# Kernel optimization log

Hardware: AMD Instinct MI355X
Metric: run time of the kernel (lower is better)

The kernel has to match this reference:

```python
import jax, jax.numpy as jnp
import numpy as np

V, D, H = 32000, 256, 1024
B, T = 64, 512


def setup_inputs() -> dict:
    key = jax.random.key(0)
    k1, k2, k3, k4 = jax.random.split(key, 4)
    inputs = jax.random.randint(k1, (B, T), 0, V, dtype=jnp.int64 if jax.config.jax_enable_x64 else jnp.int32)
    hidden_state = jnp.zeros((B, H), dtype=jnp.float32)
    embedding = jax.random.normal(k2, (V, D), dtype=jnp.float32) * 0.05
    kernel = jax.random.normal(k3, (D, 3 * H), dtype=jnp.float32) * (1.0 / np.sqrt(D))
    rec_kernel = jax.random.normal(k4, (H, 3 * H), dtype=jnp.float32) * (1.0 / np.sqrt(H))
    bias = jnp.zeros((2, 3 * H), dtype=jnp.float32)  # [input_bias; recurrent_bias] (reset_after=True)
    return {"inputs": inputs, "hidden_state": hidden_state, "embedding": embedding,
            "kernel": kernel, "rec_kernel": rec_kernel, "bias": bias}


def reference(inputs, hidden_state, embedding, kernel, rec_kernel, bias):
    # Embedding lookup: [B,T] -> [B,T,D]
    x = embedding[inputs]
    # Precompute all input projections for the whole sequence: [B,T,3H]
    x_proj = jnp.einsum('btd,dh->bth', x, kernel) + bias[0]

    def step(h, xp_t):
        # Keras GRU, reset_after=True (cuDNN-compatible gate ordering z,r,h)
        rec = h @ rec_kernel + bias[1]              # [B,3H]
        xz, xr, xh = jnp.split(xp_t, 3, axis=-1)
        rz, rr, rh = jnp.split(rec, 3, axis=-1)
        z = jax.nn.sigmoid(xz + rz)
        r = jax.nn.sigmoid(xr + rr)
        hh = jnp.tanh(xh + r * rh)
        h_new = z * h + (1.0 - z) * hh
        return h_new, h_new

    state, outs = jax.lax.scan(step, hidden_state, jnp.swapaxes(x_proj, 0, 1))
    outputs = jnp.swapaxes(outs, 0, 1)  # [B,T,H]
    return outputs, state
```

## Files before the change

kernel.cpp:

```cpp
#include <hip/hip_runtime.h>

#define Bb 64
#define Tt 512
#define Dd 256
#define Hh 1024
#define G3 3072

#define FLAG_BYTES 4096
#define HF_OFF     FLAG_BYTES

typedef __attribute__((ext_vector_type(8))) __bf16 bf16x8;
typedef __attribute__((ext_vector_type(4))) float f32x4;
typedef __attribute__((ext_vector_type(2))) unsigned long long u64x2;

static __device__ __forceinline__ f32x4 mfma16(bf16x8 a, bf16x8 b, f32x4 c){
    return __builtin_amdgcn_mfma_f32_16x16x32_bf16(a, b, c, 0, 0, 0);
}
static __device__ __forceinline__ unsigned short bfbits(__bf16 v){
    return __builtin_bit_cast(unsigned short, v);
}

__device__ __forceinline__ void gatherX(__bf16* sxh, __bf16* sxl,
                                        const int* inp, const float* emb,
                                        int m, int t, int lt)
{
    int row = lt >> 3, c8 = lt & 7;
    int grow = m*16 + row;
    int tok = inp[grow*Tt + t];
    const float* er = emb + (long)tok * Dd;
    int swz = (row & 7) << 4;
    #pragma unroll
    for (int qq = 0; qq < 8; ++qq){
        int c = c8 + qq*8;
        float4 v = *(const float4*)(er + c*4);
        int boff = row*512 + ((c*8) ^ swz);
        float vv[4] = {v.x, v.y, v.z, v.w};
        unsigned long long Hp = 0, Lp = 0;
        #pragma unroll
        for (int ee = 0; ee < 4; ++ee){
            __bf16 hb = (__bf16)vv[ee];
            __bf16 lb = (__bf16)(vv[ee] - (float)hb);
            Hp |= (unsigned long long)bfbits(hb) << (16*ee);
            Lp |= (unsigned long long)bfbits(lb) << (16*ee);
        }
        *(unsigned long long*)((char*)sxh + boff) = Hp;
        *(unsigned long long*)((char*)sxl + boff) = Lp;
    }
}

extern "C" __global__ void __launch_bounds__(512, 2)
gru_persist(const int* __restrict__ inp, const float* __restrict__ hid,
            const float* __restrict__ emb, const float* __restrict__ kern,
            const float* __restrict__ reck, const float* __restrict__ bias,
            float* __restrict__ out, unsigned char* __restrict__ ws)
{
    __shared__ __bf16 sX[2][2][16*256];
    __shared__ float  sTile[8][4][256];

    const int tid  = threadIdx.x;
    const int wid  = tid >> 6;
    const int lane = tid & 63;
    const int blk  = blockIdx.x;
    const int m = blk & 3;
    const int n = blk >> 2;

    unsigned int* flags = (unsigned int*)ws;
    unsigned char* hF = ws + HF_OFF;

    const int e    = wid;
    const int kgrp = lane >> 4;
    const int arow = lane & 15;

    bf16x8 Bh[3][4], Bl[3][4], XBh[3], XBl[3];
    #pragma unroll
    for (int g = 0; g < 3; ++g){
        #pragma unroll
        for (int ks = 0; ks < 4; ++ks){
            bf16x8 bh, bl;
            #pragma unroll
            for (int i = 0; i < 8; ++i){
                int k = e*128 + ks*32 + kgrp*8 + i;
                float f = reck[k*G3 + g*1024 + n*16 + arow];
                __bf16 h = (__bf16)f;
                bh[i] = h;
                bl[i] = (__bf16)(f - (float)h);
            }
            Bh[g][ks] = bh; Bl[g][ks] = bl;
        }
        {
            bf16x8 bh, bl;
            #pragma unroll
            for (int i = 0; i < 8; ++i){
                int k = e*32 + kgrp*8 + i;
                float f = kern[k*G3 + g*1024 + n*16 + arow];
                __bf16 h = (__bf16)f;
                bh[i] = h;
                bl[i] = (__bf16)(f - (float)h);
            }
            XBh[g] = bh; XBl[g] = bl;
        }
    }

    float cbz = 0.f, cbr = 0.f, cb0h = 0.f, cb1h = 0.f;
    size_t pubOff0 = 0, pubOff1 = 0;
    if (tid < 256){
        int row = tid >> 4, j = tid & 15;
        int c = n*16 + j;
        cbz  = bias[c]        + bias[G3 + c];
        cbr  = bias[1024 + c] + bias[G3 + 1024 + c];
        cb0h = bias[2048 + c];
        cb1h = bias[G3 + 2048 + c];
        int e_p = n >> 3;
        int cc  = c & 127;
        int ce  = cc & ~1;
        int ks = ce >> 5, kg = (ce >> 3) & 3, b = ce & 7;
        int plane = j & 1;
        size_t chunk = ((((size_t)m)*8 + e_p)*8 + plane*4 + ks)*64 + kg*16 + row;
        pubOff0 = chunk*16 + b*2;
        pubOff1 = ((size_t)4*8*8*64)*16 + pubOff0;
    }

    float hloc = 0.f;
    if (tid < 256){
        int row = tid >> 4, jj = tid & 15;
        int grow = m*16 + row, gcol = n*16 + jj;
        float hv = hid[grow*Hh + gcol];
        hloc = hv;
        __bf16 hb = (__bf16)hv;
        __bf16 lb = (__bf16)(hv - (float)hb);
        unsigned int hu = (unsigned int)bfbits(hb);
        unsigned int lu = (unsigned int)bfbits(lb);
        unsigned int ph = __shfl_xor(hu, 1);
        unsigned int pl = __shfl_xor(lu, 1);
        unsigned int val = ((jj & 1) == 0) ? ((ph << 16) | hu) : ((lu << 16) | pl);
        __hip_atomic_store((unsigned int*)(hF + pubOff0), val,
                           __ATOMIC_RELAXED, __HIP_MEMORY_SCOPE_AGENT);
        __asm__ __volatile__("s_waitcnt vmcnt(0)" ::: "memory");
        if ((tid & 63) == 0)
            __hip_atomic_store(&flags[(m*64 + n)*4 + wid], 1u,
                               __ATOMIC_RELAXED, __HIP_MEMORY_SCOPE_AGENT);
    } else if (wid >= 6){
        gatherX(&sX[0][0][0], &sX[0][1][0], inp, emb, m, 0, tid - 384);
    }
    __syncthreads();

    const int swz = (arow & 7) << 4;
    auto ldA = [&](const __bf16* base, int rowStrideB, int kbyte) -> bf16x8 {
        int off = (arow*rowStrideB + (kbyte ^ swz)) >> 1;
        return *(const bf16x8*)(base + off);
    };

    for (int t = 0; t < Tt; ++t){
        const int p = t & 1, qb = p ^ 1;

        {
            unsigned int need = (unsigned)(t + 1);
            unsigned int* fp = &flags[(m*64 + e*8 + ((lane >> 2) & 7))*4 + (lane & 3)];
            int spin = 0;
            for (;;){
                unsigned int v = __hip_atomic_load(fp, __ATOMIC_RELAXED, __HIP_MEMORY_SCOPE_AGENT);
                if (__all(v >= need)) break;
                if (++spin > 50000000) break;
                __builtin_amdgcn_s_sleep(1);
            }
            __asm__ __volatile__("" ::: "memory");
        }

        f32x4 acc0 = {0,0,0,0}, acc1 = {0,0,0,0};
        f32x4 acc2 = {0,0,0,0}, acc3 = {0,0,0,0};
        {
            const unsigned long long* bw = (const unsigned long long*)hF
                + (((size_t)p*4 + m)*8 + e)*1024 + lane*2;
            unsigned long long va[8], vb[8];
            #pragma unroll
            for (int i = 0; i < 8; ++i){
                va[i] = __hip_atomic_load(bw + i*128,     __ATOMIC_RELAXED, __HIP_MEMORY_SCOPE_AGENT);
                vb[i] = __hip_atomic_load(bw + i*128 + 1, __ATOMIC_RELAXED, __HIP_MEMORY_SCOPE_AGENT);
            }
            #pragma unroll
            for (int ks = 0; ks < 4; ++ks){
                bf16x8 Ah = __builtin_bit_cast(bf16x8, (u64x2){va[ks],   vb[ks]});
                bf16x8 Al = __builtin_bit_cast(bf16x8, (u64x2){va[4+ks], vb[4+ks]});
                acc0 = mfma16(Ah, Bh[0][ks], acc0);
                acc1 = mfma16(Ah, Bh[1][ks], acc1);
                acc2 = mfma16(Ah, Bh[2][ks], acc2);
                acc0 = mfma16(Ah, Bl[0][ks], acc0);
                acc1 = mfma16(Ah, Bl[1][ks], acc1);
                acc2 = mfma16(Ah, Bl[2][ks], acc2);
                acc0 = mfma16(Al, Bh[0][ks], acc0);
                acc1 = mfma16(Al, Bh[1][ks], acc1);
                acc2 = mfma16(Al, Bh[2][ks], acc2);
            }
            {
                int kbx = e*64 + kgrp*16;
                bf16x8 Ah = ldA(&sX[p][0][0], 512, kbx);
                bf16x8 Al = ldA(&sX[p][1][0], 512, kbx);
                acc0 = mfma16(Ah, XBh[0], acc0);
                acc1 = mfma16(Ah, XBh[1], acc1);
                acc3 = mfma16(Ah, XBh[2], acc3);
                acc0 = mfma16(Ah, XBl[0], acc0);
                acc1 = mfma16(Ah, XBl[1], acc1);
                acc3 = mfma16(Ah, XBl[2], acc3);
                acc0 = mfma16(Al, XBh[0], acc0);
                acc1 = mfma16(Al, XBh[1], acc1);
                acc3 = mfma16(Al, XBh[2], acc3);
            }
            #pragma unroll
            for (int r = 0; r < 4; ++r){
                int ix = (kgrp*4 + r)*16 + arow;
                sTile[e][0][ix] = acc0[r];
                sTile[e][1][ix] = acc1[r];
                sTile[e][2][ix] = acc2[r];
                sTile[e][3][ix] = acc3[r];
            }
        }
        __syncthreads();

        if (tid < 256){
            int row = tid >> 4, jj = tid & 15;
            int ix = row*16 + jj;
            float pz = cbz, pr = cbr, rh = cb1h, xh = cb0h;
            #pragma unroll
            for (int w = 0; w < 8; ++w){
                pz += sTile[w][0][ix];
                pr += sTile[w][1][ix];
                rh += sTile[w][2][ix];
                xh += sTile[w][3][ix];
            }
            float z  = 1.f/(1.f + expf(-pz));
            float r  = 1.f/(1.f + expf(-pr));
            float hhat = tanhf(xh + r*rh);
            int grow = m*16 + row, gcol = n*16 + jj;
            float hn = z*hloc + (1.f - z)*hhat;
            hloc = hn;
            __bf16 nh = (__bf16)hn;
            __bf16 nl = (__bf16)(hn - (float)nh);
            unsigned int hu = (unsigned int)bfbits(nh);
            unsigned int lu = (unsigned int)bfbits(nl);
            unsigned int ph = __shfl_xor(hu, 1);
            unsigned int pl = __shfl_xor(lu, 1);
            unsigned int val = ((jj & 1) == 0) ? ((ph << 16) | hu) : ((lu << 16) | pl);
            __hip_atomic_store((unsigned int*)(hF + (qb ? pubOff1 : pubOff0)), val,
                               __ATOMIC_RELAXED, __HIP_MEMORY_SCOPE_AGENT);
            __asm__ __volatile__("s_waitcnt vmcnt(0)" ::: "memory");
            if ((tid & 63) == 0)
                __hip_atomic_store(&flags[(m*64 + n)*4 + wid], (unsigned)(t + 2),
                                   __ATOMIC_RELAXED, __HIP_MEMORY_SCOPE_AGENT);
            out[((long)grow*Tt + t)*Hh + gcol] = hn;
            if (t == Tt - 1)
                out[(long)Bb*Tt*Hh + grow*Hh + gcol] = hn;
        } else if (wid >= 6){
            if (t + 1 < Tt)
                gatherX(&sX[qb][0][0], &sX[qb][1][0], inp, emb, m, t + 1, tid - 384);
        }
        __syncthreads();
    }
}

extern "C" void kernel_launch(void* const* d_in, const int* in_sizes, int n_in,
                              void* d_out, int out_size, void* d_ws, size_t ws_size,
                              hipStream_t stream)
{
    (void)in_sizes; (void)n_in; (void)out_size; (void)ws_size;
    const int*   inp  = (const int*)  d_in[0];
    const float* hid  = (const float*)d_in[1];
    const float* emb  = (const float*)d_in[2];
    const float* kern = (const float*)d_in[3];
    const float* reck = (const float*)d_in[4];
    const float* bias = (const float*)d_in[5];
    float* out = (float*)d_out;
    unsigned char* ws = (unsigned char*)d_ws;

    hipMemsetAsync(ws, 0, FLAG_BYTES, stream);

    void* args[] = {(void*)&inp, (void*)&hid, (void*)&emb, (void*)&kern,
                    (void*)&reck, (void*)&bias, (void*)&out, (void*)&ws};
    hipLaunchCooperativeKernel((void*)gru_persist, dim3(256), dim3(512),
                               args, 0, stream);
}
```

Baseline: 1.951 ms.

## Embed step-parity tags in published hidden-state words, removing separate flag barrier

Replaces the per-wave flag array and spin-on-flags handshake with 2-bit sequence tags packed into the low bits of each published bf16 low-part value, so consumers spin directly on the data loads until every word carries the expected tag. This drops the store-then-waitcnt-then-flag round trip and the extra flag polling latency on each recurrent step. The input-projection MFMAs are also moved ahead of the spin so they overlap with waiting. The cost is losing two mantissa bits of the low bf16 correction term, plus repeated reloading of the full data tile while spinning, and a larger workspace memset.

```diff
diff --git a/kernel.cpp b/kernel.cpp
--- a/kernel.cpp
+++ b/kernel.cpp
@@ -6,18 +6,25 @@
 #define Hh 1024
 #define G3 3072
 
-#define FLAG_BYTES 4096
-#define HF_OFF     FLAG_BYTES
+#define HF_BYTES (512*1024)
+#define PLANE_U32 65536
+#define PLANE_U64 32768
 
 typedef __attribute__((ext_vector_type(8))) __bf16 bf16x8;
 typedef __attribute__((ext_vector_type(4))) float f32x4;
-typedef __attribute__((ext_vector_type(2))) unsigned long long u64x2;
+typedef __attribute__((ext_vector_type(4))) unsigned int u32x4;
 
 static __device__ __forceinline__ f32x4 mfma16(bf16x8 a, bf16x8 b, f32x4 c){
     return __builtin_amdgcn_mfma_f32_16x16x32_bf16(a, b, c, 0, 0, 0);
 }
 static __device__ __forceinline__ unsigned short bfbits(__bf16 v){
     return __builtin_bit_cast(unsigned short, v);
+}
+
+static __device__ __forceinline__ size_t hfIdx(int p, int m, int c, int row){
+    int e = c >> 7, ks = (c >> 5) & 3, kg = (c >> 3) & 3, i = c & 7;
+    int lane = kg*16 + row;
+    return (size_t)((((p*4 + m)*8 + e)*4 + ks)*64 + lane)*8 + i;
 }
 
 __device__ __forceinline__ void gatherX(__bf16* sxh, __bf16* sxl,
@@ -64,8 +71,7 @@
     const int m = blk & 3;
     const int n = blk >> 2;
 
-    unsigned int* flags = (unsigned int*)ws;
-    unsigned char* hF = ws + HF_OFF;
+    unsigned int* hF = (unsigned int*)ws;
 
     const int e    = wid;
     const int kgrp = lane >> 4;
@@ -102,7 +108,7 @@
     }
 
     float cbz = 0.f, cbr = 0.f, cb0h = 0.f, cb1h = 0.f;
-    size_t pubOff0 = 0, pubOff1 = 0;
+    size_t pubIdx = 0;
     if (tid < 256){
         int row = tid >> 4, j = tid & 15;
         int c = n*16 + j;
@@ -110,15 +116,10 @@
         cbr  = bias[1024 + c] + bias[G3 + 1024 + c];
         cb0h = bias[2048 + c];
         cb1h = bias[G3 + 2048 + c];
-        int e_p = n >> 3;
-        int cc  = c & 127;
-        int ce  = cc & ~1;
-        int ks = ce >> 5, kg = (ce >> 3) & 3, b = ce & 7;
-        int plane = j & 1;
-        size_t chunk = ((((size_t)m)*8 + e_p)*8 + plane*4 + ks)*64 + kg*16 + row;
-        pubOff0 = chunk*16 + b*2;
-        pubOff1 = ((size_t)4*8*8*64)*16 + pubOff0;
-    }
+        pubIdx = hfIdx(0, m, c, row);
+    }
+
+    const size_t cbase = (size_t)(((m*8 + e)*4)*64 + lane)*4;
 
     float hloc = 0.f;
     if (tid < 256){
@@ -128,17 +129,9 @@
         hloc = hv;
         __bf16 hb = (__bf16)hv;
         __bf16 lb = (__bf16)(hv - (float)hb);
-        unsigned int hu = (unsigned int)bfbits(hb);
-        unsigned int lu = (unsigned int)bfbits(lb);
-        unsigned int ph = __shfl_xor(hu, 1);
-        unsigned int pl = __shfl_xor(lu, 1);
-        unsigned int val = ((jj & 1) == 0) ? ((ph << 16) | hu) : ((lu << 16) | pl);
-        __hip_atomic_store((unsigned int*)(hF + pubOff0), val,
-                           __ATOMIC_RELAXED, __HIP_MEMORY_SCOPE_AGENT);
-        __asm__ __volatile__("s_waitcnt vmcnt(0)" ::: "memory");
-        if ((tid & 63) == 0)
-            __hip_atomic_store(&flags[(m*64 + n)*4 + wid], 1u,
-                               __ATOMIC_RELAXED, __HIP_MEMORY_SCOPE_AGENT);
+        unsigned int val = (unsigned int)bfbits(hb)
+                         | ((((unsigned int)bfbits(lb) & ~3u) | 1u) << 16);
+        __hip_atomic_store(&hF[pubIdx], val, __ATOMIC_RELAXED, __HIP_MEMORY_SCOPE_AGENT);
     } else if (wid >= 6){
         gatherX(&sX[0][0][0], &sX[0][1][0], inp, emb, m, 0, tid - 384);
     }
@@ -152,67 +145,76 @@
 
     for (int t = 0; t < Tt; ++t){
         const int p = t & 1, qb = p ^ 1;
+        const unsigned long long pat =
+            (unsigned long long)((unsigned)(t + 1) & 3u) * 0x0001000000010000ULL;
+
+        f32x4 acc0 = {0,0,0,0}, acc1 = {0,0,0,0};
+        f32x4 acc2 = {0,0,0,0}, acc3 = {0,0,0,0};
 
         {
-            unsigned int need = (unsigned)(t + 1);
-            unsigned int* fp = &flags[(m*64 + e*8 + ((lane >> 2) & 7))*4 + (lane & 3)];
+            int kbx = e*64 + kgrp*16;
+            bf16x8 Ah = ldA(&sX[p][0][0], 512, kbx);
+            bf16x8 Al = ldA(&sX[p][1][0], 512, kbx);
+            acc0 = mfma16(Ah, XBh[0], acc0);
+            acc1 = mfma16(Ah, XBh[1], acc1);
+            acc3 = mfma16(Ah, XBh[2], acc3);
+            acc0 = mfma16(Ah, XBl[0], acc0);
+            acc1 = mfma16(Ah, XBl[1], acc1);
+            acc3 = mfma16(Ah, XBl[2], acc3);
+            acc0 = mfma16(Al, XBh[0], acc0);
+            acc1 = mfma16(Al, XBh[1], acc1);
+            acc3 = mfma16(Al, XBh[2], acc3);
+        }
+
+        unsigned long long v[16];
+        {
+            const unsigned long long* hb64 = (const unsigned long long*)hF;
+            const size_t base = cbase + (size_t)p*PLANE_U64;
             int spin = 0;
             for (;;){
-                unsigned int v = __hip_atomic_load(fp, __ATOMIC_RELAXED, __HIP_MEMORY_SCOPE_AGENT);
-                if (__all(v >= need)) break;
-                if (++spin > 50000000) break;
-                __builtin_amdgcn_s_sleep(1);
-            }
-            __asm__ __volatile__("" ::: "memory");
-        }
-
-        f32x4 acc0 = {0,0,0,0}, acc1 = {0,0,0,0};
-        f32x4 acc2 = {0,0,0,0}, acc3 = {0,0,0,0};
-        {
-            const unsigned long long* bw = (const unsigned long long*)hF
-                + (((size_t)p*4 + m)*8 + e)*1024 + lane*2;
-            unsigned long long va[8], vb[8];
-            #pragma unroll
-            for (int i = 0; i < 8; ++i){
-                va[i] = __hip_atomic_load(bw + i*128,     __ATOMIC_RELAXED, __HIP_MEMORY_SCOPE_AGENT);
-                vb[i] = __hip_atomic_load(bw + i*128 + 1, __ATOMIC_RELAXED, __HIP_MEMORY_SCOPE_AGENT);
-            }
-            #pragma unroll
-            for (int ks = 0; ks < 4; ++ks){
-                bf16x8 Ah = __builtin_bit_cast(bf16x8, (u64x2){va[ks],   vb[ks]});
-                bf16x8 Al = __builtin_bit_cast(bf16x8, (u64x2){va[4+ks], vb[4+ks]});
-                acc0 = mfma16(Ah, Bh[0][ks], acc0);
-                acc1 = mfma16(Ah, Bh[1][ks], acc1);
-                acc2 = mfma16(Ah, Bh[2][ks], acc2);
-                acc0 = mfma16(Ah, Bl[0][ks], acc0);
-                acc1 = mfma16(Ah, Bl[1][ks], acc1);
-                acc2 = mfma16(Ah, Bl[2][ks], acc2);
-                acc0 = mfma16(Al, Bh[0][ks], acc0);
-                acc1 = mfma16(Al, Bh[1][ks], acc1);
-                acc2 = mfma16(Al, Bh[2][ks], acc2);
-            }
-            {
-                int kbx = e*64 + kgrp*16;
-                bf16x8 Ah = ldA(&sX[p][0][0], 512, kbx);
-                bf16x8 Al = ldA(&sX[p][1][0], 512, kbx);
-                acc0 = mfma16(Ah, XBh[0], acc0);
-                acc1 = mfma16(Ah, XBh[1], acc1);
-                acc3 = mfma16(Ah, XBh[2], acc3);
-                acc0 = mfma16(Ah, XBl[0], acc0);
-                acc1 = mfma16(Ah, XBl[1], acc1);
-                acc3 = mfma16(Ah, XBl[2], acc3);
-                acc0 = mfma16(Al, XBh[0], acc0);
-                acc1 = mfma16(Al, XBh[1], acc1);
-                acc3 = mfma16(Al, XBh[2], acc3);
-            }
-            #pragma unroll
-            for (int r = 0; r < 4; ++r){
-                int ix = (kgrp*4 + r)*16 + arow;
-                sTile[e][0][ix] = acc0[r];
-                sTile[e][1][ix] = acc1[r];
-                sTile[e][2][ix] = acc2[r];
-                sTile[e][3][ix] = acc3[r];
-            }
+                #pragma unroll
+                for (int ks = 0; ks < 4; ++ks)
+                    #pragma unroll
+                    for (int j = 0; j < 4; ++j)
+                        v[ks*4 + j] = __hip_atomic_load(hb64 + base + ks*256 + j,
+                                          __ATOMIC_RELAXED, __HIP_MEMORY_SCOPE_AGENT);
+                unsigned long long bad = 0;
+                #pragma unroll
+                for (int i = 0; i < 16; ++i)
+                    bad |= (v[i] ^ pat) & 0x0003000000030000ULL;
+                if (__all(bad == 0)) break;
+                if (++spin > 1000000) break;
+            }
+        }
+        #pragma unroll
+        for (int ks = 0; ks < 4; ++ks){
+            unsigned int ah[4], al[4];
+            #pragma unroll
+            for (int j = 0; j < 4; ++j){
+                unsigned int a = (unsigned int)v[ks*4 + j];
+                unsigned int b = (unsigned int)(v[ks*4 + j] >> 32);
+                ah[j] = (a & 0xFFFFu) | (b << 16);
+                al[j] = (a >> 16) | (b & 0xFFFF0000u);
+            }
+            bf16x8 Ah = __builtin_bit_cast(bf16x8, (u32x4){ah[0], ah[1], ah[2], ah[3]});
+            bf16x8 Al = __builtin_bit_cast(bf16x8, (u32x4){al[0], al[1], al[2], al[3]});
+            acc0 = mfma16(Ah, Bh[0][ks], acc0);
+            acc1 = mfma16(Ah, Bh[1][ks], acc1);
+            acc2 = mfma16(Ah, Bh[2][ks], acc2);
+            acc0 = mfma16(Ah, Bl[0][ks], acc0);
+            acc1 = mfma16(Ah, Bl[1][ks], acc1);
+            acc2 = mfma16(Ah, Bl[2][ks], acc2);
+            acc0 = mfma16(Al, Bh[0][ks], acc0);
+            acc1 = mfma16(Al, Bh[1][ks], acc1);
+            acc2 = mfma16(Al, Bh[2][ks], acc2);
+        }
+        #pragma unroll
+        for (int r = 0; r < 4; ++r){
+            int ix = (kgrp*4 + r)*16 + arow;
+            sTile[e][0][ix] = acc0[r];
+            sTile[e][1][ix] = acc1[r];
+            sTile[e][2][ix] = acc2[r];
+            sTile[e][3][ix] = acc3[r];
         }
         __syncthreads();
 
@@ -235,17 +237,10 @@
             hloc = hn;
             __bf16 nh = (__bf16)hn;
             __bf16 nl = (__bf16)(hn - (float)nh);
-            unsigned int hu = (unsigned int)bfbits(nh);
-            unsigned int lu = (unsigned int)bfbits(nl);
-            unsigned int ph = __shfl_xor(hu, 1);
-            unsigned int pl = __shfl_xor(lu, 1);
-            unsigned int val = ((jj & 1) == 0) ? ((ph << 16) | hu) : ((lu << 16) | pl);
-            __hip_atomic_store((unsigned int*)(hF + (qb ? pubOff1 : pubOff0)), val,
+            unsigned int val = (unsigned int)bfbits(nh)
+                | ((((unsigned int)bfbits(nl) & ~3u) | ((unsigned)(t + 2) & 3u)) << 16);
+            __hip_atomic_store(&hF[pubIdx + (size_t)qb*PLANE_U32], val,
                                __ATOMIC_RELAXED, __HIP_MEMORY_SCOPE_AGENT);
-            __asm__ __volatile__("s_waitcnt vmcnt(0)" ::: "memory");
-            if ((tid & 63) == 0)
-                __hip_atomic_store(&flags[(m*64 + n)*4 + wid], (unsigned)(t + 2),
-                                   __ATOMIC_RELAXED, __HIP_MEMORY_SCOPE_AGENT);
             out[((long)grow*Tt + t)*Hh + gcol] = hn;
             if (t == Tt - 1)
                 out[(long)Bb*Tt*Hh + grow*Hh + gcol] = hn;
@@ -271,7 +266,7 @@
     float* out = (float*)d_out;
     unsigned char* ws = (unsigned char*)d_ws;
 
-    hipMemsetAsync(ws, 0, FLAG_BYTES, stream);
+    hipMemsetAsync(ws, 0, HF_BYTES, stream);
 
     void* args[] = {(void*)&inp, (void*)&hid, (void*)&emb, (void*)&kern,
                     (void*)&reck, (void*)&bias, (void*)&out, (void*)&ws};
```

Result: no change. 1.945 ms (-0.3%).
